# Kernel optimization log

Measured on AMD Instinct MI355X. Metric: run time of the kernel, lower is better.

Reference implementation:

```python
import jax, jax.numpy as jnp
import numpy as np

# model dims (match init_kwargs)
D = 1024      # input_dim
H = 4096      # hidden_dim
O = 1024      # expert_output_dim
E = 8         # num_experts
K = 2         # top_k


def setup_inputs() -> dict:
    key = jax.random.key(0)
    ks = jax.random.split(key, 8)
    B, S = 2, 2048
    x = jax.random.normal(ks[0], (B, S, D), dtype=jnp.float32)
    s = 0.02
    Wr = jax.random.normal(ks[1], (D, E), dtype=jnp.float32) * s
    br = jnp.zeros((E,), dtype=jnp.float32)
    W1 = jax.random.normal(ks[2], (E, D, H), dtype=jnp.float32) * s
    b1 = jnp.zeros((E, H), dtype=jnp.float32)
    W2 = jax.random.normal(ks[3], (E, H, O), dtype=jnp.float32) * s
    b2 = jnp.zeros((E, O), dtype=jnp.float32)
    return {"x": x, "Wr": Wr, "br": br, "W1": W1, "b1": b1, "W2": W2, "b2": b2}


def reference(x, Wr, br, W1, b1, W2, b2):
    B, S, _ = x.shape
    T = B * S
    xf = x.reshape(T, D)                                  # [T, D]
    logits = xf @ Wr + br                                 # [T, E]
    topk_logits, topk_idx = jax.lax.top_k(logits, K)      # [T, K]
    gates = jax.nn.softmax(topk_logits, axis=1)           # softmax over the K selected logits
    # scatter gates into a dense [T, E] matrix (top-k indices are unique per token)
    dense_gates = jnp.zeros((T, E), dtype=logits.dtype).at[
        jnp.arange(T)[:, None], topk_idx
    ].set(gates)
    # run every expert FFN densely, then combine with (mostly-zero) gates
    h = jax.nn.relu(jnp.einsum('td,edh->teh', xf, W1) + b1)   # [T, E, H]
    y = jnp.einsum('teh,eho->teo', h, W2) + b2                # [T, E, O]
    out = jnp.einsum('te,teo->to', dense_gates, y)            # [T, O]
    return out.reshape(B, S, O)
```

## Files before the change

kernel.cpp:

```cpp
#include <hip/hip_runtime.h>
#include <stdint.h>

#define KD 1024
#define KH 4096
#define KO 1024
#define KE 8
#define KT 4096

typedef unsigned short u16;
typedef __bf16 bf16x8 __attribute__((ext_vector_type(8)));
typedef unsigned short ushort8 __attribute__((ext_vector_type(8)));
typedef float floatx4 __attribute__((ext_vector_type(4)));

__device__ __forceinline__ u16 f2bf(float f) {
  unsigned u = __float_as_uint(f);
  u += 0x7fffu + ((u >> 16) & 1u);
  return (u16)(u >> 16);
}

__global__ void cvt_x_k(const float* __restrict__ x, u16* __restrict__ xbf) {
  int i = blockIdx.x * blockDim.x + threadIdx.x;
  float4 v = ((const float4*)x)[i];
  union { u16 u[4]; uint2 v2; } o;
  o.u[0] = f2bf(v.x); o.u[1] = f2bf(v.y); o.u[2] = f2bf(v.z); o.u[3] = f2bf(v.w);
  ((uint2*)xbf)[i] = o.v2;
}

__global__ void transpose_k(const float* __restrict__ in, u16* __restrict__ out,
                            int R, int C) {
  __shared__ float tile[32][33];
  const int e = blockIdx.z;
  const float* I = in + (size_t)e * R * C;
  u16* Oo = out + (size_t)e * R * C;
  const int c0 = blockIdx.x * 32, r0 = blockIdx.y * 32;
  const int tx = threadIdx.x, ty = threadIdx.y;
#pragma unroll
  for (int i = 0; i < 4; i++) {
    int r = r0 + ty + i * 8;
    tile[ty + i * 8][tx] = I[(size_t)r * C + c0 + tx];
  }
  __syncthreads();
#pragma unroll
  for (int i = 0; i < 4; i++) {
    int c = c0 + ty + i * 8;
    Oo[(size_t)c * R + r0 + tx] = f2bf(tile[tx][ty + i * 8]);
  }
}

__global__ void router_k(const float* __restrict__ x, const float* __restrict__ Wr,
                         const float* __restrict__ br, int* __restrict__ cnt,
                         int* __restrict__ tok, float* __restrict__ gat) {
  const int t = blockIdx.x;
  const int lane = threadIdx.x;
  const float* xr = x + (size_t)t * KD;
  double acc[KE];
#pragma unroll
  for (int e = 0; e < KE; e++) acc[e] = 0.0;
  for (int i = lane; i < KD; i += 64) {
    float xv = xr[i];
    const float* wr = Wr + i * KE;
#pragma unroll
    for (int e = 0; e < KE; e++) acc[e] += (double)xv * (double)wr[e];
  }
#pragma unroll
  for (int e = 0; e < KE; e++) {
#pragma unroll
    for (int m = 32; m > 0; m >>= 1) acc[e] += __shfl_xor(acc[e], m, 64);
  }
  if (lane == 0) {
    float l[KE];
#pragma unroll
    for (int e = 0; e < KE; e++) l[e] = (float)acc[e] + br[e];
    int i0 = 0;
#pragma unroll
    for (int e = 1; e < KE; e++) if (l[e] > l[i0]) i0 = e;
    int i1 = -1;
#pragma unroll
    for (int e = 0; e < KE; e++) {
      if (e == i0) continue;
      if (i1 < 0 || l[e] > l[i1]) i1 = e;
    }
    float g0 = 1.0f / (1.0f + expf(l[i1] - l[i0]));
    float g1 = 1.0f - g0;
    int p0 = atomicAdd(&cnt[i0], 1);
    tok[(i0 << 12) + p0] = t; gat[(i0 << 12) + p0] = g0;
    int p1 = atomicAdd(&cnt[i1], 1);
    tok[(i1 << 12) + p1] = t; gat[(i1 << 12) + p1] = g1;
  }
}

__global__ void offsets_k(const int* __restrict__ cnt, int* __restrict__ offs) {
  if (threadIdx.x == 0 && blockIdx.x == 0) {
    int s = 0;
#pragma unroll
    for (int e = 0; e < KE; e++) { offs[e] = s; s += cnt[e]; }
  }
}

__global__ __launch_bounds__(256) void gemm1_k(
    const u16* __restrict__ xbf, const u16* __restrict__ w1t,
    const float* __restrict__ b1, const int* __restrict__ cnt,
    const int* __restrict__ offs, const int* __restrict__ tok,
    u16* __restrict__ hbuf) {
  const int e = blockIdx.z;
  const int me = cnt[e];
  const int m0 = blockIdx.y * 128;
  if (m0 >= me) return;
  const int n0 = blockIdx.x * 128;
  const int oe = offs[e];
  const int* tk = tok + (e << 12);

  __shared__ u16 As[128 * 32];
  __shared__ u16 Bs[128 * 32];

  const int tid = threadIdx.x;
  const int lane = tid & 63;
  const int w = tid >> 6;
  const int wm = w >> 1, wn = w & 1;

  const int srow = tid >> 1;
  const int scol = (tid & 1) << 4;
  const int arow = m0 + srow;
  const int atok = (arow < me) ? tk[arow] : 0;
  const u16* ap = xbf + ((size_t)atok << 10) + scol;
  const u16* bp = w1t + ((size_t)e << 22) + ((size_t)(n0 + srow) << 10) + scol;
  u16* asw = &As[srow * 32 + scol];
  u16* bsw = &Bs[srow * 32 + scol];

  floatx4 acc[4][4] = {};
  const int fr = lane & 15;
  const int kq = (lane >> 4) << 3;

  for (int kt = 0; kt < KD / 32; ++kt) {
    ushort8 a0 = *(const ushort8*)(ap + kt * 32);
    ushort8 a1 = *(const ushort8*)(ap + kt * 32 + 8);
    ushort8 b0 = *(const ushort8*)(bp + kt * 32);
    ushort8 b1v = *(const ushort8*)(bp + kt * 32 + 8);
    __syncthreads();
    *(ushort8*)asw = a0;
    *(ushort8*)(asw + 8) = a1;
    *(ushort8*)bsw = b0;
    *(ushort8*)(bsw + 8) = b1v;
    __syncthreads();
    bf16x8 af[4], bfr[4];
#pragma unroll
    for (int i = 0; i < 4; i++) {
      af[i]  = __builtin_bit_cast(bf16x8, *(const ushort8*)&As[(wm * 64 + i * 16 + fr) * 32 + kq]);
      bfr[i] = __builtin_bit_cast(bf16x8, *(const ushort8*)&Bs[(wn * 64 + i * 16 + fr) * 32 + kq]);
    }
#pragma unroll
    for (int mi = 0; mi < 4; mi++)
#pragma unroll
      for (int ni = 0; ni < 4; ni++)
        acc[mi][ni] = __builtin_amdgcn_mfma_f32_16x16x32_bf16(af[mi], bfr[ni], acc[mi][ni], 0, 0, 0);
  }

  const int q = lane >> 4;
#pragma unroll
  for (int ni = 0; ni < 4; ni++) {
    const int gcol = n0 + wn * 64 + ni * 16 + fr;
    const float bb = b1[(e << 12) + gcol];
#pragma unroll
    for (int mi = 0; mi < 4; mi++) {
#pragma unroll
      for (int r = 0; r < 4; r++) {
        const int gr = m0 + wm * 64 + mi * 16 + q * 4 + r;
        if (gr < me) {
          float v = fmaxf(acc[mi][ni][r] + bb, 0.0f);
          hbuf[((size_t)(oe + gr) << 12) + gcol] = f2bf(v);
        }
      }
    }
  }
}

__global__ __launch_bounds__(256) void gemm2_k(
    const u16* __restrict__ hbuf, const u16* __restrict__ w2t,
    const float* __restrict__ b2, const int* __restrict__ cnt,
    const int* __restrict__ offs, const int* __restrict__ tok,
    const float* __restrict__ gat, float* __restrict__ out) {
  const int e = blockIdx.z;
  const int me = cnt[e];
  const int m0 = blockIdx.y * 128;
  if (m0 >= me) return;
  const int n0 = blockIdx.x * 128;
  const int oe = offs[e];
  const int* tk = tok + (e << 12);

  __shared__ u16 As[128 * 32];
  __shared__ u16 Bs[128 * 32];

  const int tid = threadIdx.x;
  const int lane = tid & 63;
  const int w = tid >> 6;
  const int wm = w >> 1, wn = w & 1;

  const int srow = tid >> 1;
  const int scol = (tid & 1) << 4;
  const int arow = m0 + srow;
  const int slot = oe + ((arow < me) ? arow : 0);
  const u16* ap = hbuf + ((size_t)slot << 12) + scol;
  const u16* bp = w2t + ((size_t)e << 22) + ((size_t)(n0 + srow) << 12) + scol;
  u16* asw = &As[srow * 32 + scol];
  u16* bsw = &Bs[srow * 32 + scol];

  floatx4 acc[4][4] = {};
  const int fr = lane & 15;
  const int kq = (lane >> 4) << 3;

  for (int kt = 0; kt < KH / 32; ++kt) {
    ushort8 a0 = *(const ushort8*)(ap + kt * 32);
    ushort8 a1 = *(const ushort8*)(ap + kt * 32 + 8);
    ushort8 b0 = *(const ushort8*)(bp + kt * 32);
    ushort8 b1v = *(const ushort8*)(bp + kt * 32 + 8);
    __syncthreads();
    *(ushort8*)asw = a0;
    *(ushort8*)(asw + 8) = a1;
    *(ushort8*)bsw = b0;
    *(ushort8*)(bsw + 8) = b1v;
    __syncthreads();
    bf16x8 af[4], bfr[4];
#pragma unroll
    for (int i = 0; i < 4; i++) {
      af[i]  = __builtin_bit_cast(bf16x8, *(const ushort8*)&As[(wm * 64 + i * 16 + fr) * 32 + kq]);
      bfr[i] = __builtin_bit_cast(bf16x8, *(const ushort8*)&Bs[(wn * 64 + i * 16 + fr) * 32 + kq]);
    }
#pragma unroll
    for (int mi = 0; mi < 4; mi++)
#pragma unroll
      for (int ni = 0; ni < 4; ni++)
        acc[mi][ni] = __builtin_amdgcn_mfma_f32_16x16x32_bf16(af[mi], bfr[ni], acc[mi][ni], 0, 0, 0);
  }

  const int q = lane >> 4;
  float bb[4];
#pragma unroll
  for (int ni = 0; ni < 4; ni++) bb[ni] = b2[(e << 10) + n0 + wn * 64 + ni * 16 + fr];
#pragma unroll
  for (int mi = 0; mi < 4; mi++) {
#pragma unroll
    for (int r = 0; r < 4; r++) {
      const int gr = m0 + wm * 64 + mi * 16 + q * 4 + r;
      if (gr < me) {
        const int tt = tk[gr];
        const float g = gat[(e << 12) + gr];
        float* orow = out + ((size_t)tt << 10);
#pragma unroll
        for (int ni = 0; ni < 4; ni++) {
          const int gcol = n0 + wn * 64 + ni * 16 + fr;
          atomicAdd(orow + gcol, (acc[mi][ni][r] + bb[ni]) * g);
        }
      }
    }
  }
}

extern "C" void kernel_launch(void* const* d_in, const int* in_sizes, int n_in,
                              void* d_out, int out_size, void* d_ws, size_t ws_size,
                              hipStream_t stream) {
  const float* x  = (const float*)d_in[0];
  const float* Wr = (const float*)d_in[1];
  const float* br = (const float*)d_in[2];
  const float* W1 = (const float*)d_in[3];
  const float* b1 = (const float*)d_in[4];
  const float* W2 = (const float*)d_in[5];
  const float* b2 = (const float*)d_in[6];
  float* out = (float*)d_out;

  char* ws = (char*)d_ws;
  size_t p = 0;
  auto alloc = [&](size_t bytes) {
    void* r = ws + p;
    p = (p + bytes + 255) & ~(size_t)255;
    return r;
  };
  int*   cnt  = (int*)alloc(KE * 4);
  int*   offs = (int*)alloc(KE * 4);
  int*   tok  = (int*)alloc((size_t)KE * KT * 4);
  float* gat  = (float*)alloc((size_t)KE * KT * 4);
  u16*   xbf  = (u16*)alloc((size_t)KT * KD * 2);
  u16*   w1t  = (u16*)alloc((size_t)KE * KD * KH * 2);
  u16*   w2t  = (u16*)alloc((size_t)KE * KH * KO * 2);
  u16*   hbuf = (u16*)alloc((size_t)2 * KT * KH * 2);

  hipMemsetAsync(out, 0, (size_t)KT * KO * 4, stream);
  hipMemsetAsync(cnt, 0, KE * 4, stream);

  cvt_x_k<<<(KT * KD / 4) / 256, 256, 0, stream>>>(x, xbf);
  transpose_k<<<dim3(KH / 32, KD / 32, KE), dim3(32, 8), 0, stream>>>(W1, w1t, KD, KH);
  transpose_k<<<dim3(KO / 32, KH / 32, KE), dim3(32, 8), 0, stream>>>(W2, w2t, KH, KO);
  router_k<<<KT, 64, 0, stream>>>(x, Wr, br, cnt, tok, gat);
  offsets_k<<<1, 64, 0, stream>>>(cnt, offs);
  gemm1_k<<<dim3(KH / 128, KT / 128, KE), 256, 0, stream>>>(xbf, w1t, b1, cnt, offs, tok, hbuf);
  gemm2_k<<<dim3(KO / 128, KT / 128, KE), 256, 0, stream>>>(hbuf, w2t, b2, cnt, offs, tok, gat, out);
}
```

Measured before the change: 739.9 us.

## Use direct global-to-LDS loads, split-K gemm2, deterministic per-expert bucketing

The GEMM kernels now stage A and B tiles with global_load_lds, so data goes straight from global memory into shared memory without passing through registers. gemm2 splits the hidden dimension into two halves, doubling the number of blocks, and combines the halves through the existing atomic adds, with the bias added only by the first half. The router no longer does atomics: it writes per-token expert pairs, and a new bucket kernel builds each expert's token list with a prefix scan. Trade-offs are a full waitcnt stall on every k-step with no double buffering, twice as many atomic adds into the output, and one extra kernel launch.

```diff
diff --git a/kernel.cpp b/kernel.cpp
--- a/kernel.cpp
+++ b/kernel.cpp
@@ -16,6 +16,12 @@
   unsigned u = __float_as_uint(f);
   u += 0x7fffu + ((u >> 16) & 1u);
   return (u16)(u >> 16);
+}
+
+__device__ __forceinline__ void glds16(const u16* g, u16* l) {
+  __builtin_amdgcn_global_load_lds(
+      (const __attribute__((address_space(1))) unsigned int*)(g),
+      (__attribute__((address_space(3))) unsigned int*)(l), 16, 0, 0);
 }
 
 __global__ void cvt_x_k(const float* __restrict__ x, u16* __restrict__ xbf) {
@@ -48,8 +54,8 @@
 }
 
 __global__ void router_k(const float* __restrict__ x, const float* __restrict__ Wr,
-                         const float* __restrict__ br, int* __restrict__ cnt,
-                         int* __restrict__ tok, float* __restrict__ gat) {
+                         const float* __restrict__ br, int* __restrict__ eidx,
+                         float2* __restrict__ gpair) {
   const int t = blockIdx.x;
   const int lane = threadIdx.x;
   const float* xr = x + (size_t)t * KD;
@@ -81,11 +87,48 @@
       if (i1 < 0 || l[e] > l[i1]) i1 = e;
     }
     float g0 = 1.0f / (1.0f + expf(l[i1] - l[i0]));
-    float g1 = 1.0f - g0;
-    int p0 = atomicAdd(&cnt[i0], 1);
-    tok[(i0 << 12) + p0] = t; gat[(i0 << 12) + p0] = g0;
-    int p1 = atomicAdd(&cnt[i1], 1);
-    tok[(i1 << 12) + p1] = t; gat[(i1 << 12) + p1] = g1;
+    eidx[t] = i0 | (i1 << 4);
+    gpair[t] = make_float2(g0, 1.0f - g0);
+  }
+}
+
+__global__ __launch_bounds__(256) void bucket_k(const int* __restrict__ eidx,
+                                                const float2* __restrict__ gp,
+                                                int* __restrict__ cnt,
+                                                int* __restrict__ tok,
+                                                float* __restrict__ gat) {
+  const int e = blockIdx.x;
+  const int tid = threadIdx.x;
+  const int t0 = tid * 16;
+  int f[16]; float g[16]; int c = 0;
+#pragma unroll
+  for (int j = 0; j < 16; j++) {
+    int pk = eidx[t0 + j];
+    float2 gg = gp[t0 + j];
+    int h0 = ((pk & 15) == e);
+    int h1 = (((pk >> 4) & 15) == e);
+    f[j] = h0 | h1;
+    g[j] = h0 ? gg.x : gg.y;
+    c += f[j];
+  }
+  __shared__ int sc[256];
+  sc[tid] = c;
+  __syncthreads();
+  for (int d = 1; d < 256; d <<= 1) {
+    int add = (tid >= d) ? sc[tid - d] : 0;
+    __syncthreads();
+    sc[tid] += add;
+    __syncthreads();
+  }
+  int base = sc[tid] - c;
+  if (tid == 0) cnt[e] = sc[255];
+#pragma unroll
+  for (int j = 0; j < 16; j++) {
+    if (f[j]) {
+      tok[(e << 12) + base] = t0 + j;
+      gat[(e << 12) + base] = g[j];
+      base++;
+    }
   }
 }
 
@@ -118,29 +161,33 @@
   const int w = tid >> 6;
   const int wm = w >> 1, wn = w & 1;
 
-  const int srow = tid >> 1;
-  const int scol = (tid & 1) << 4;
-  const int arow = m0 + srow;
-  const int atok = (arow < me) ? tk[arow] : 0;
-  const u16* ap = xbf + ((size_t)atok << 10) + scol;
-  const u16* bp = w1t + ((size_t)e << 22) + ((size_t)(n0 + srow) << 10) + scol;
-  u16* asw = &As[srow * 32 + scol];
-  u16* bsw = &Bs[srow * 32 + scol];
+  const int rr = lane >> 2;
+  const int cc = (lane & 3) << 3;
+  const int ar0 = m0 + w * 32 + rr;
+  const int ar1 = ar0 + 16;
+  const int ta0 = (ar0 < me) ? tk[ar0] : 0;
+  const int ta1 = (ar1 < me) ? tk[ar1] : 0;
+  const u16* ga0 = xbf + ((size_t)ta0 << 10) + cc;
+  const u16* ga1 = xbf + ((size_t)ta1 << 10) + cc;
+  const int br0 = n0 + w * 32 + rr;
+  const u16* gb0 = w1t + ((size_t)e << 22) + ((size_t)br0 << 10) + cc;
+  const u16* gb1 = gb0 + (16 << 10);
+  u16* la0 = &As[(w * 32) * 32] + lane * 8;
+  u16* la1 = la0 + 512;
+  u16* lb0 = &Bs[(w * 32) * 32] + lane * 8;
+  u16* lb1 = lb0 + 512;
 
   floatx4 acc[4][4] = {};
   const int fr = lane & 15;
   const int kq = (lane >> 4) << 3;
 
   for (int kt = 0; kt < KD / 32; ++kt) {
-    ushort8 a0 = *(const ushort8*)(ap + kt * 32);
-    ushort8 a1 = *(const ushort8*)(ap + kt * 32 + 8);
-    ushort8 b0 = *(const ushort8*)(bp + kt * 32);
-    ushort8 b1v = *(const ushort8*)(bp + kt * 32 + 8);
-    __syncthreads();
-    *(ushort8*)asw = a0;
-    *(ushort8*)(asw + 8) = a1;
-    *(ushort8*)bsw = b0;
-    *(ushort8*)(bsw + 8) = b1v;
+    __syncthreads();
+    glds16(ga0 + kt * 32, la0);
+    glds16(ga1 + kt * 32, la1);
+    glds16(gb0 + kt * 32, lb0);
+    glds16(gb1 + kt * 32, lb1);
+    __builtin_amdgcn_s_waitcnt(0);
     __syncthreads();
     bf16x8 af[4], bfr[4];
 #pragma unroll
@@ -183,7 +230,9 @@
   const int me = cnt[e];
   const int m0 = blockIdx.y * 128;
   if (m0 >= me) return;
-  const int n0 = blockIdx.x * 128;
+  const int ks = blockIdx.x & 1;
+  const int n0 = (blockIdx.x >> 1) * 128;
+  const int k0 = ks * (KH / 2);
   const int oe = offs[e];
   const int* tk = tok + (e << 12);
 
@@ -195,29 +244,33 @@
   const int w = tid >> 6;
   const int wm = w >> 1, wn = w & 1;
 
-  const int srow = tid >> 1;
-  const int scol = (tid & 1) << 4;
-  const int arow = m0 + srow;
-  const int slot = oe + ((arow < me) ? arow : 0);
-  const u16* ap = hbuf + ((size_t)slot << 12) + scol;
-  const u16* bp = w2t + ((size_t)e << 22) + ((size_t)(n0 + srow) << 12) + scol;
-  u16* asw = &As[srow * 32 + scol];
-  u16* bsw = &Bs[srow * 32 + scol];
+  const int rr = lane >> 2;
+  const int cc = (lane & 3) << 3;
+  const int ar0 = m0 + w * 32 + rr;
+  const int ar1 = ar0 + 16;
+  const int sl0 = oe + ((ar0 < me) ? ar0 : 0);
+  const int sl1 = oe + ((ar1 < me) ? ar1 : 0);
+  const u16* ga0 = hbuf + ((size_t)sl0 << 12) + k0 + cc;
+  const u16* ga1 = hbuf + ((size_t)sl1 << 12) + k0 + cc;
+  const int br0 = n0 + w * 32 + rr;
+  const u16* gb0 = w2t + ((size_t)e << 22) + ((size_t)br0 << 12) + k0 + cc;
+  const u16* gb1 = gb0 + (16 << 12);
+  u16* la0 = &As[(w * 32) * 32] + lane * 8;
+  u16* la1 = la0 + 512;
+  u16* lb0 = &Bs[(w * 32) * 32] + lane * 8;
+  u16* lb1 = lb0 + 512;
 
   floatx4 acc[4][4] = {};
   const int fr = lane & 15;
   const int kq = (lane >> 4) << 3;
 
-  for (int kt = 0; kt < KH / 32; ++kt) {
-    ushort8 a0 = *(const ushort8*)(ap + kt * 32);
-    ushort8 a1 = *(const ushort8*)(ap + kt * 32 + 8);
-    ushort8 b0 = *(const ushort8*)(bp + kt * 32);
-    ushort8 b1v = *(const ushort8*)(bp + kt * 32 + 8);
-    __syncthreads();
-    *(ushort8*)asw = a0;
-    *(ushort8*)(asw + 8) = a1;
-    *(ushort8*)bsw = b0;
-    *(ushort8*)(bsw + 8) = b1v;
+  for (int kt = 0; kt < KH / 2 / 32; ++kt) {
+    __syncthreads();
+    glds16(ga0 + kt * 32, la0);
+    glds16(ga1 + kt * 32, la1);
+    glds16(gb0 + kt * 32, lb0);
+    glds16(gb1 + kt * 32, lb1);
+    __builtin_amdgcn_s_waitcnt(0);
     __syncthreads();
     bf16x8 af[4], bfr[4];
 #pragma unroll
@@ -235,7 +288,8 @@
   const int q = lane >> 4;
   float bb[4];
 #pragma unroll
-  for (int ni = 0; ni < 4; ni++) bb[ni] = b2[(e << 10) + n0 + wn * 64 + ni * 16 + fr];
+  for (int ni = 0; ni < 4; ni++)
+    bb[ni] = (ks == 0) ? b2[(e << 10) + n0 + wn * 64 + ni * 16 + fr] : 0.0f;
 #pragma unroll
   for (int mi = 0; mi < 4; mi++) {
 #pragma unroll
@@ -274,23 +328,25 @@
     p = (p + bytes + 255) & ~(size_t)255;
     return r;
   };
-  int*   cnt  = (int*)alloc(KE * 4);
-  int*   offs = (int*)alloc(KE * 4);
-  int*   tok  = (int*)alloc((size_t)KE * KT * 4);
-  float* gat  = (float*)alloc((size_t)KE * KT * 4);
-  u16*   xbf  = (u16*)alloc((size_t)KT * KD * 2);
-  u16*   w1t  = (u16*)alloc((size_t)KE * KD * KH * 2);
-  u16*   w2t  = (u16*)alloc((size_t)KE * KH * KO * 2);
-  u16*   hbuf = (u16*)alloc((size_t)2 * KT * KH * 2);
+  int*    cnt   = (int*)alloc(KE * 4);
+  int*    offs  = (int*)alloc(KE * 4);
+  int*    eidx  = (int*)alloc((size_t)KT * 4);
+  float2* gpair = (float2*)alloc((size_t)KT * 8);
+  int*    tok   = (int*)alloc((size_t)KE * KT * 4);
+  float*  gat   = (float*)alloc((size_t)KE * KT * 4);
+  u16*    xbf   = (u16*)alloc((size_t)KT * KD * 2);
+  u16*    w1t   = (u16*)alloc((size_t)KE * KD * KH * 2);
+  u16*    w2t   = (u16*)alloc((size_t)KE * KH * KO * 2);
+  u16*    hbuf  = (u16*)alloc((size_t)2 * KT * KH * 2);
 
   hipMemsetAsync(out, 0, (size_t)KT * KO * 4, stream);
-  hipMemsetAsync(cnt, 0, KE * 4, stream);
 
   cvt_x_k<<<(KT * KD / 4) / 256, 256, 0, stream>>>(x, xbf);
   transpose_k<<<dim3(KH / 32, KD / 32, KE), dim3(32, 8), 0, stream>>>(W1, w1t, KD, KH);
   transpose_k<<<dim3(KO / 32, KH / 32, KE), dim3(32, 8), 0, stream>>>(W2, w2t, KH, KO);
-  router_k<<<KT, 64, 0, stream>>>(x, Wr, br, cnt, tok, gat);
+  router_k<<<KT, 64, 0, stream>>>(x, Wr, br, eidx, gpair);
+  bucket_k<<<KE, 256, 0, stream>>>(eidx, gpair, cnt, tok, gat);
   offsets_k<<<1, 64, 0, stream>>>(cnt, offs);
   gemm1_k<<<dim3(KH / 128, KT / 128, KE), 256, 0, stream>>>(xbf, w1t, b1, cnt, offs, tok, hbuf);
-  gemm2_k<<<dim3(KO / 128, KT / 128, KE), 256, 0, stream>>>(hbuf, w2t, b2, cnt, offs, tok, gat, out);
-}
+  gemm2_k<<<dim3(2 * KO / 128, KT / 128, KE), 256, 0, stream>>>(hbuf, w2t, b2, cnt, offs, tok, gat, out);
+}
```

New measurement: 620.4 us. 16.2% less time.
